# Optimization experiments

Measured on AMD Instinct MI355X. Metric: run time of the kernel, lower is better.

## Reference

```python
import jax, jax.numpy as jnp
import numpy as np

B, S, H = 128, 512, 512

def _xavier(key, shape):
    fan_in, fan_out = shape[1], shape[0]
    limit = float(np.sqrt(6.0 / (fan_in + fan_out)))
    return jax.random.uniform(key, shape, jnp.float32, -limit, limit)

def setup_inputs() -> dict:
    key = jax.random.key(0)
    k1, k2, k3, k4, k5 = jax.random.split(key, 5)
    return {
        "h": jax.random.normal(k1, (B, S, H), jnp.float32),
        "x": jax.random.normal(k2, (B, S, H), jnp.float32),
        "Ve": _xavier(k3, (1, H)),
        "U1": _xavier(k4, (H, 2 * H)),
        "U2": _xavier(k5, (H, H)),
    }

def reference(h, x, Ve, U1, U2):
    # h: [B,S,H], x: [B,S,H]
    h_last = h[:, -1, :]                      # [B,H]
    U1a, U1b = U1[:, :U1.shape[0]], U1[:, U1.shape[0]:]  # each [H,H]
    # u1 = concat(h_t, h_last) @ U1.T, vectorized over t
    u1 = jnp.einsum('bsh,kh->bsk', h, U1a) + jnp.einsum('bh,kh->bk', h_last, U1b)[:, None, :]
    u2 = jnp.einsum('bsh,kh->bsk', x, U2)
    u = jnp.tanh(u1 + u2)                     # [B,S,H]
    e = jnp.einsum('bsk,k->bs', u, Ve[0])     # [B,S]
    alpha = jax.nn.softmax(e, axis=1)         # [B,S]
    context = jnp.einsum('bs,bsh->bh', alpha, h)
    return context
```

## Files before the change

### kernel.cpp

```cpp
#include <hip/hip_runtime.h>
#include <cstdint>
#include <cstddef>


typedef _Float16 h8 __attribute__((ext_vector_type(8)));
typedef float    f4 __attribute__((ext_vector_type(4)));

#define GLOAD16(g, l)                                                          \
  __builtin_amdgcn_global_load_lds(                                            \
      (const __attribute__((address_space(1))) void*)(g),                      \
      (__attribute__((address_space(3))) void*)(l), 16, 0, 0)

#define PIPE_BARRIER(N)                                                        \
  do {                                                                         \
    asm volatile("s_waitcnt vmcnt(" #N ") lgkmcnt(0)\n\ts_barrier" ::: "memory"); \
    __builtin_amdgcn_sched_barrier(0);                                         \
  } while (0)

__global__ void bsetup_kernel(const float* __restrict__ U1, const float* __restrict__ U2,
                              _Float16* __restrict__ Bws) {
  int g = blockIdx.x * 256 + threadIdx.x;
  int s  = g & 7;
  int r  = (g >> 3) & 127;
  int kt = (g >> 10) & 15;
  int nt = g >> 14;
  int n = nt * 128 + r;
  int k = kt * 64 + ((s ^ (r & 7)) << 3);
  const float* p = (k < 512) ? (U1 + (size_t)n * 1024 + k)
                             : (U2 + (size_t)n * 512 + (k - 512));
  float4 a = *(const float4*)p;
  float4 b = *(const float4*)(p + 4);
  _Float16 hv[8];
  hv[0]=(_Float16)a.x; hv[1]=(_Float16)a.y; hv[2]=(_Float16)a.z; hv[3]=(_Float16)a.w;
  hv[4]=(_Float16)b.x; hv[5]=(_Float16)b.y; hv[6]=(_Float16)b.z; hv[7]=(_Float16)b.w;
  *(uint4*)(Bws + ((size_t)g << 3)) = *(uint4*)hv;
}

__global__ void bias_kernel(const float* __restrict__ hT, const float* __restrict__ U1,
                            float* __restrict__ bias) {
  const int b = blockIdx.x, t = threadIdx.x;
  const int l = t & 63, w = t >> 6;
  __shared__ float4 hl[128];
  if (t < 128) hl[t] = *(const float4*)(hT + ((size_t)b * 512 + 511) * 512 + t * 4);
  __syncthreads();
  for (int n = w; n < 512; n += 4) {
    const float4* ur = (const float4*)(U1 + (size_t)n * 1024 + 512);
    float4 u0 = ur[l],      u1 = ur[l + 64];
    float4 h0 = hl[l],      h1 = hl[l + 64];
    float s = u0.x*h0.x + u0.y*h0.y + u0.z*h0.z + u0.w*h0.w
            + u1.x*h1.x + u1.y*h1.y + u1.z*h1.z + u1.w*h1.w;
#pragma unroll
    for (int d = 1; d < 64; d <<= 1) s += __shfl_xor(s, d, 64);
    if (l == 0) bias[(size_t)b * 512 + n] = s;
  }
}

__global__ __launch_bounds__(256, 2)
void gemm_kernel(const float* __restrict__ hT, const float* __restrict__ xT,
                 const _Float16* __restrict__ Bws, const float* __restrict__ bias,
                 const float* __restrict__ Ve, float* __restrict__ e) {
  const int bid  = ((int)blockIdx.x & 7) * 256 + ((int)blockIdx.x >> 3);
  const int bm   = bid >> 2;
  const int nt   = bid & 3;
  const int row0 = bm * 128;
  const int bb   = row0 >> 9;
  const int t    = threadIdx.x;
  const int l    = t & 63;
  const int wv   = t >> 6;
  const int wm   = wv >> 1, wn = wv & 1;
  const int l15  = l & 15, lhi = l >> 4;

  __shared__ __align__(16) _Float16 Asm[2][8192];
  __shared__ __align__(16) _Float16 Bsm[2][8192];

  const int arow = t >> 4;
  const int aslt = t & 15;

  f4 areg[2][8];

  auto LOADA = [&](int buf, int k2) {
    const float* p = ((k2 < 8) ? hT : xT) + (size_t)row0 * 512 + (k2 & 7) * 64 + aslt * 4;
#pragma unroll
    for (int q = 0; q < 8; ++q)
      areg[buf][q] = *(const f4*)(p + (size_t)(q * 16 + arow) * 512);
  };
  auto GLOADB = [&](int c, int k2) {
    const _Float16* tb = Bws + ((size_t)(nt * 16 + k2) << 13);
#pragma unroll
    for (int j = 0; j < 4; ++j)
      GLOAD16(tb + ((j * 256 + wv * 64 + l) << 3), &Bsm[c][(j * 256 + wv * 64) << 3]);
  };
  auto WRITEA = [&](int c, int buf) {
#pragma unroll
    for (int q = 0; q < 8; ++q) {
      const f4 v = areg[buf][q];
      _Float16 hv[4];
      hv[0]=(_Float16)v[0]; hv[1]=(_Float16)v[1]; hv[2]=(_Float16)v[2]; hv[3]=(_Float16)v[3];
      const int r = q * 16 + arow;
      *(uint2*)&Asm[c][r * 64 + (((aslt >> 1) ^ (r & 7)) << 3) + ((aslt & 1) << 2)] = *(uint2*)hv;
    }
  };

  f4 acc[4][4];
#pragma unroll
  for (int mf = 0; mf < 4; ++mf)
#pragma unroll
    for (int nf = 0; nf < 4; ++nf)
      acc[mf][nf] = (f4){0.f, 0.f, 0.f, 0.f};

  GLOADB(0, 0);
  LOADA(0, 0);
  WRITEA(0, 0);
  LOADA(1, 1);
  PIPE_BARRIER(8);

#pragma unroll
  for (int kt = 0; kt < 16; ++kt) {
    const int c = kt & 1;
    if (kt < 15) GLOADB(c ^ 1, kt + 1);
    if (kt < 14) LOADA(c, kt + 2);
    __builtin_amdgcn_sched_barrier(0);
#pragma unroll
    for (int kk = 0; kk < 2; ++kk) {
      h8 af[4], bf[4];
#pragma unroll
      for (int mf = 0; mf < 4; ++mf) {
        const int rA = wm * 64 + mf * 16 + l15;
        af[mf] = *(const h8*)&Asm[c][rA * 64 + ((((kk << 2) + lhi) ^ (rA & 7)) << 3)];
      }
#pragma unroll
      for (int nf = 0; nf < 4; ++nf) {
        const int rB = wn * 64 + nf * 16 + l15;
        bf[nf] = *(const h8*)&Bsm[c][rB * 64 + ((((kk << 2) + lhi) ^ (rB & 7)) << 3)];
      }
#pragma unroll
      for (int mf = 0; mf < 4; ++mf)
#pragma unroll
        for (int nf = 0; nf < 4; ++nf)
          acc[mf][nf] = __builtin_amdgcn_mfma_f32_16x16x32_f16(af[mf], bf[nf], acc[mf][nf], 0, 0, 0);
    }
    if (kt < 15) WRITEA(c ^ 1, c ^ 1);
    if (kt < 14)       { PIPE_BARRIER(8); }
    else if (kt == 14) { PIPE_BARRIER(0); }
  }

  float vev[4], biasv[4];
#pragma unroll
  for (int nf = 0; nf < 4; ++nf) {
    int cidx = nt * 128 + wn * 64 + nf * 16 + l15;
    vev[nf]   = Ve[cidx];
    biasv[nf] = bias[(size_t)bb * 512 + cidx];
  }
#pragma unroll
  for (int mf = 0; mf < 4; ++mf) {
#pragma unroll
    for (int j = 0; j < 4; ++j) {
      float s = 0.f;
#pragma unroll
      for (int nf = 0; nf < 4; ++nf)
        s += tanhf(acc[mf][nf][j] + biasv[nf]) * vev[nf];
#pragma unroll
      for (int m = 1; m < 16; m <<= 1) s += __shfl_xor(s, m, 64);
      if (l15 == 0) atomicAdd(&e[row0 + wm * 64 + mf * 16 + lhi * 4 + j], s);
    }
  }
}

__global__ void softmax_kernel(float* __restrict__ e) {
  const int b = blockIdx.x, t = threadIdx.x;
  float* row = e + (size_t)b * 512;
  float v0 = row[t], v1 = row[t + 256];
  float m = fmaxf(v0, v1);
#pragma unroll
  for (int d = 1; d < 64; d <<= 1) m = fmaxf(m, __shfl_xor(m, d, 64));
  __shared__ float r1[4], r2[4];
  if ((t & 63) == 0) r1[t >> 6] = m;
  __syncthreads();
  m = fmaxf(fmaxf(r1[0], r1[1]), fmaxf(r1[2], r1[3]));
  float e0 = expf(v0 - m), e1 = expf(v1 - m);
  float s = e0 + e1;
#pragma unroll
  for (int d = 1; d < 64; d <<= 1) s += __shfl_xor(s, d, 64);
  if ((t & 63) == 0) r2[t >> 6] = s;
  __syncthreads();
  s = r2[0] + r2[1] + r2[2] + r2[3];
  float inv = 1.0f / s;
  row[t]       = e0 * inv;
  row[t + 256] = e1 * inv;
}

__global__ __launch_bounds__(512)
void ctx_kernel(const float* __restrict__ hT, const float* __restrict__ alpha,
                float* __restrict__ out) {
  const int b  = blockIdx.x >> 2;
  const int sc = blockIdx.x & 3;
  const int hd = threadIdx.x;
  __shared__ float al[128];
  if (threadIdx.x < 128) al[threadIdx.x] = alpha[(size_t)b * 512 + sc * 128 + threadIdx.x];
  __syncthreads();
  const float* hp = hT + ((size_t)b * 512 + sc * 128) * 512 + hd;
  float acc = 0.f;
#pragma unroll 4
  for (int s = 0; s < 128; ++s) acc += al[s] * hp[(size_t)s * 512];
  atomicAdd(&out[b * 512 + hd], acc);
}

extern "C" void kernel_launch(void* const* d_in, const int* in_sizes, int n_in,
                              void* d_out, int out_size, void* d_ws, size_t ws_size,
                              hipStream_t stream) {
  const float* h  = (const float*)d_in[0];
  const float* x  = (const float*)d_in[1];
  const float* Ve = (const float*)d_in[2];
  const float* U1 = (const float*)d_in[3];
  const float* U2 = (const float*)d_in[4];
  float* out = (float*)d_out;

  _Float16* Bws  = (_Float16*)d_ws;
  float*    bias = (float*)((char*)d_ws + (1u << 20));
  float*    e    = (float*)((char*)d_ws + (1u << 20) + (256u << 10));
  if (ws_size < ((1u << 20) + (512u << 10))) return;

  hipMemsetAsync(e, 0, 65536 * sizeof(float), stream);
  hipMemsetAsync(d_out, 0, 65536 * sizeof(float), stream);

  bsetup_kernel<<<256, 256, 0, stream>>>(U1, U2, Bws);
  bias_kernel<<<128, 256, 0, stream>>>(h, U1, bias);
  gemm_kernel<<<2048, 256, 0, stream>>>(h, x, Bws, bias, Ve, e);
  softmax_kernel<<<128, 256, 0, stream>>>(e);
  ctx_kernel<<<512, 512, 0, stream>>>(h, e, out);
}
```

Before: 224.6 us.

## Switch GEMM to 32x32x16 MFMA with single-buffered register-staged LDS tiles

The fused attention-score GEMM now uses 32x32x16 f16 MFMA instructions with a 2x2 accumulator tile per wave in place of 4x4 tiles of 16x16x32. LDS drops to a single buffer with both A and B staged through registers, replacing the direct global-to-LDS loads for B. Occupancy is raised to 3 blocks per CU via launch bounds, and the B workspace layout is simplified to plain K-tile-major order with the swizzle applied on the LDS write. The aim is fewer LDS fragment reads per MFMA and more resident waves, at the cost of an extra barrier per K step and less overlap between LDS writes and compute.

```diff
diff --git a/kernel.cpp b/kernel.cpp
--- a/kernel.cpp
+++ b/kernel.cpp
@@ -3,37 +3,31 @@
 #include <cstddef>
 
 
-typedef _Float16 h8 __attribute__((ext_vector_type(8)));
-typedef float    f4 __attribute__((ext_vector_type(4)));
-
-#define GLOAD16(g, l)                                                          \
-  __builtin_amdgcn_global_load_lds(                                            \
-      (const __attribute__((address_space(1))) void*)(g),                      \
-      (__attribute__((address_space(3))) void*)(l), 16, 0, 0)
-
-#define PIPE_BARRIER(N)                                                        \
+typedef _Float16 h8     __attribute__((ext_vector_type(8)));
+typedef float    f4     __attribute__((ext_vector_type(4)));
+typedef float    f32x16 __attribute__((ext_vector_type(16)));
+
+#define LBAR()                                                                 \
   do {                                                                         \
-    asm volatile("s_waitcnt vmcnt(" #N ") lgkmcnt(0)\n\ts_barrier" ::: "memory"); \
+    asm volatile("s_waitcnt lgkmcnt(0)\n\ts_barrier" ::: "memory");            \
     __builtin_amdgcn_sched_barrier(0);                                         \
   } while (0)
 
 __global__ void bsetup_kernel(const float* __restrict__ U1, const float* __restrict__ U2,
                               _Float16* __restrict__ Bws) {
   int g = blockIdx.x * 256 + threadIdx.x;
-  int s  = g & 7;
-  int r  = (g >> 3) & 127;
-  int kt = (g >> 10) & 15;
-  int nt = g >> 14;
-  int n = nt * 128 + r;
-  int k = kt * 64 + ((s ^ (r & 7)) << 3);
-  const float* p = (k < 512) ? (U1 + (size_t)n * 1024 + k)
-                             : (U2 + (size_t)n * 512 + (k - 512));
+  int j  = g & 7;
+  int n  = (g >> 3) & 511;
+  int kt = g >> 12;
+  int k0 = kt * 64 + j * 8;
+  const float* p = (k0 < 512) ? (U1 + (size_t)n * 1024 + k0)
+                              : (U2 + (size_t)n * 512 + (k0 - 512));
   float4 a = *(const float4*)p;
   float4 b = *(const float4*)(p + 4);
   _Float16 hv[8];
   hv[0]=(_Float16)a.x; hv[1]=(_Float16)a.y; hv[2]=(_Float16)a.z; hv[3]=(_Float16)a.w;
   hv[4]=(_Float16)b.x; hv[5]=(_Float16)b.y; hv[6]=(_Float16)b.z; hv[7]=(_Float16)b.w;
-  *(uint4*)(Bws + ((size_t)g << 3)) = *(uint4*)hv;
+  *(uint4*)(Bws + (size_t)kt * 32768 + n * 64 + j * 8) = *(uint4*)hv;
 }
 
 __global__ void bias_kernel(const float* __restrict__ hT, const float* __restrict__ U1,
@@ -55,7 +49,7 @@
   }
 }
 
-__global__ __launch_bounds__(256, 2)
+__global__ __launch_bounds__(256, 3)
 void gemm_kernel(const float* __restrict__ hT, const float* __restrict__ xT,
                  const _Float16* __restrict__ Bws, const float* __restrict__ bias,
                  const float* __restrict__ Ve, float* __restrict__ e) {
@@ -68,100 +62,108 @@
   const int l    = t & 63;
   const int wv   = t >> 6;
   const int wm   = wv >> 1, wn = wv & 1;
-  const int l15  = l & 15, lhi = l >> 4;
-
-  __shared__ __align__(16) _Float16 Asm[2][8192];
-  __shared__ __align__(16) _Float16 Bsm[2][8192];
-
-  const int arow = t >> 4;
-  const int aslt = t & 15;
-
-  f4 areg[2][8];
-
-  auto LOADA = [&](int buf, int k2) {
-    const float* p = ((k2 < 8) ? hT : xT) + (size_t)row0 * 512 + (k2 & 7) * 64 + aslt * 4;
-#pragma unroll
-    for (int q = 0; q < 8; ++q)
-      areg[buf][q] = *(const f4*)(p + (size_t)(q * 16 + arow) * 512);
+  const int l31  = l & 31, khalf = l >> 5;
+
+  __shared__ __align__(16) _Float16 Asm[128 * 64];
+  __shared__ __align__(16) _Float16 Bsm[128 * 64];
+
+  f4    areg[8];
+  uint4 breg[4];
+
+  const int as = t & 15, arw = t >> 4;
+  const int bs = t & 7,  brw = t >> 3;
+
+  auto LOADA = [&](int kt) {
+    const float* p = ((kt < 8) ? hT : xT)
+                   + (size_t)(row0 + arw) * 512 + (kt & 7) * 64 + as * 4;
+#pragma unroll
+    for (int q = 0; q < 8; ++q) areg[q] = *(const f4*)(p + (size_t)q * 16 * 512);
   };
-  auto GLOADB = [&](int c, int k2) {
-    const _Float16* tb = Bws + ((size_t)(nt * 16 + k2) << 13);
-#pragma unroll
-    for (int j = 0; j < 4; ++j)
-      GLOAD16(tb + ((j * 256 + wv * 64 + l) << 3), &Bsm[c][(j * 256 + wv * 64) << 3]);
+  auto LOADB = [&](int kt) {
+    const _Float16* p = Bws + (size_t)kt * 32768 + (nt * 128 + brw) * 64 + bs * 8;
+#pragma unroll
+    for (int q = 0; q < 4; ++q) breg[q] = *(const uint4*)(p + q * 32 * 64);
   };
-  auto WRITEA = [&](int c, int buf) {
+  auto WRITE = [&]() {
 #pragma unroll
     for (int q = 0; q < 8; ++q) {
-      const f4 v = areg[buf][q];
+      const int R = arw + q * 16;
+      const f4 v = areg[q];
       _Float16 hv[4];
       hv[0]=(_Float16)v[0]; hv[1]=(_Float16)v[1]; hv[2]=(_Float16)v[2]; hv[3]=(_Float16)v[3];
-      const int r = q * 16 + arow;
-      *(uint2*)&Asm[c][r * 64 + (((aslt >> 1) ^ (r & 7)) << 3) + ((aslt & 1) << 2)] = *(uint2*)hv;
+      *(uint2*)&Asm[R * 64 + (((as >> 1) ^ (R & 7)) << 3) + ((as & 1) << 2)] = *(uint2*)hv;
+    }
+#pragma unroll
+    for (int q = 0; q < 4; ++q) {
+      const int N = brw + q * 32;
+      *(uint4*)&Bsm[N * 64 + ((bs ^ (N & 7)) << 3)] = breg[q];
     }
   };
 
-  f4 acc[4][4];
-#pragma unroll
-  for (int mf = 0; mf < 4; ++mf)
-#pragma unroll
-    for (int nf = 0; nf < 4; ++nf)
-      acc[mf][nf] = (f4){0.f, 0.f, 0.f, 0.f};
-
-  GLOADB(0, 0);
-  LOADA(0, 0);
-  WRITEA(0, 0);
-  LOADA(1, 1);
-  PIPE_BARRIER(8);
+  f32x16 acc[2][2];
+#pragma unroll
+  for (int mi = 0; mi < 2; ++mi)
+#pragma unroll
+    for (int ni = 0; ni < 2; ++ni)
+      acc[mi][ni] = (f32x16)(0.f);
+
+  LOADA(0); LOADB(0);
+  WRITE();
+  LOADA(1); LOADB(1);
+  LBAR();
 
 #pragma unroll
   for (int kt = 0; kt < 16; ++kt) {
-    const int c = kt & 1;
-    if (kt < 15) GLOADB(c ^ 1, kt + 1);
-    if (kt < 14) LOADA(c, kt + 2);
-    __builtin_amdgcn_sched_barrier(0);
-#pragma unroll
-    for (int kk = 0; kk < 2; ++kk) {
-      h8 af[4], bf[4];
-#pragma unroll
-      for (int mf = 0; mf < 4; ++mf) {
-        const int rA = wm * 64 + mf * 16 + l15;
-        af[mf] = *(const h8*)&Asm[c][rA * 64 + ((((kk << 2) + lhi) ^ (rA & 7)) << 3)];
+#pragma unroll
+    for (int ks = 0; ks < 4; ++ks) {
+      h8 af[2], bf[2];
+      const int sl = ks * 2 + khalf;
+#pragma unroll
+      for (int mi = 0; mi < 2; ++mi) {
+        const int R = wm * 64 + mi * 32 + l31;
+        af[mi] = *(const h8*)&Asm[R * 64 + ((sl ^ (R & 7)) << 3)];
       }
 #pragma unroll
-      for (int nf = 0; nf < 4; ++nf) {
-        const int rB = wn * 64 + nf * 16 + l15;
-        bf[nf] = *(const h8*)&Bsm[c][rB * 64 + ((((kk << 2) + lhi) ^ (rB & 7)) << 3)];
+      for (int ni = 0; ni < 2; ++ni) {
+        const int R = wn * 64 + ni * 32 + l31;
+        bf[ni] = *(const h8*)&Bsm[R * 64 + ((sl ^ (R & 7)) << 3)];
       }
 #pragma unroll
-      for (int mf = 0; mf < 4; ++mf)
-#pragma unroll
-        for (int nf = 0; nf < 4; ++nf)
-          acc[mf][nf] = __builtin_amdgcn_mfma_f32_16x16x32_f16(af[mf], bf[nf], acc[mf][nf], 0, 0, 0);
-    }
-    if (kt < 15) WRITEA(c ^ 1, c ^ 1);
-    if (kt < 14)       { PIPE_BARRIER(8); }
-    else if (kt == 14) { PIPE_BARRIER(0); }
-  }
-
-  float vev[4], biasv[4];
-#pragma unroll
-  for (int nf = 0; nf < 4; ++nf) {
-    int cidx = nt * 128 + wn * 64 + nf * 16 + l15;
-    vev[nf]   = Ve[cidx];
-    biasv[nf] = bias[(size_t)bb * 512 + cidx];
-  }
-#pragma unroll
-  for (int mf = 0; mf < 4; ++mf) {
-#pragma unroll
-    for (int j = 0; j < 4; ++j) {
-      float s = 0.f;
-#pragma unroll
-      for (int nf = 0; nf < 4; ++nf)
-        s += tanhf(acc[mf][nf][j] + biasv[nf]) * vev[nf];
-#pragma unroll
-      for (int m = 1; m < 16; m <<= 1) s += __shfl_xor(s, m, 64);
-      if (l15 == 0) atomicAdd(&e[row0 + wm * 64 + mf * 16 + lhi * 4 + j], s);
+      for (int mi = 0; mi < 2; ++mi)
+#pragma unroll
+        for (int ni = 0; ni < 2; ++ni)
+          acc[mi][ni] = __builtin_amdgcn_mfma_f32_32x32x16_f16(af[mi], bf[ni], acc[mi][ni], 0, 0, 0);
+    }
+    LBAR();
+    if (kt < 15) {
+      WRITE();
+      if (kt < 14) { LOADA(kt + 2); LOADB(kt + 2); }
+      LBAR();
+    }
+  }
+
+  float vev[2], biasv[2];
+#pragma unroll
+  for (int ni = 0; ni < 2; ++ni) {
+    const int c = nt * 128 + wn * 64 + ni * 32 + l31;
+    vev[ni]   = Ve[c];
+    biasv[ni] = bias[(size_t)bb * 512 + c];
+  }
+#pragma unroll
+  for (int mi = 0; mi < 2; ++mi) {
+    float s[16];
+#pragma unroll
+    for (int r = 0; r < 16; ++r) {
+      s[r] = tanhf(acc[mi][0][r] + biasv[0]) * vev[0]
+           + tanhf(acc[mi][1][r] + biasv[1]) * vev[1];
+#pragma unroll
+      for (int d = 1; d < 32; d <<= 1) s[r] += __shfl_xor(s[r], d, 64);
+    }
+    if (l31 == 0) {
+      const int rbase = row0 + wm * 64 + mi * 32 + 4 * khalf;
+#pragma unroll
+      for (int r = 0; r < 16; ++r)
+        atomicAdd(&e[rbase + (r & 3) + 8 * (r >> 2)], s[r]);
     }
   }
 }
```

Result: slower. 355.3 us (+58.2%).
